# Optimization experiments

Hardware: AMD Instinct MI355X
Metric: run time of the kernel (lower is better)

Reference implementation:

```python
import jax, jax.numpy as jnp
import numpy as np

B, C, E, H = 4, 2048, 1024, 16
D = E // H
EPS = 1e-5

def _layernorm(x, g, b):
    mu = jnp.mean(x, axis=-1, keepdims=True)
    var = jnp.mean(jnp.square(x - mu), axis=-1, keepdims=True)
    return (x - mu) * jax.lax.rsqrt(var + EPS) * g + b

def setup_inputs() -> dict:
    key = jax.random.key(0)
    ks = jax.random.split(key, 12)
    s = 1.0 / np.sqrt(E)
    return {
        "inputs": jax.random.normal(ks[0], (B, C, E), dtype=jnp.float32),
        "Wq": jax.random.normal(ks[1], (E, E), dtype=jnp.float32) * s,
        "bq": jnp.zeros((E,), dtype=jnp.float32),
        "Wk": jax.random.normal(ks[2], (E, E), dtype=jnp.float32) * s,
        "bk": jnp.zeros((E,), dtype=jnp.float32),
        "Wv": jax.random.normal(ks[3], (E, E), dtype=jnp.float32) * s,
        "bv": jnp.zeros((E,), dtype=jnp.float32),
        "g1": jnp.ones((E,), dtype=jnp.float32),
        "beta1": jnp.zeros((E,), dtype=jnp.float32),
        "g2": jnp.ones((E,), dtype=jnp.float32),
        "beta2": jnp.zeros((E,), dtype=jnp.float32),
        "W1": jax.random.normal(ks[4], (E, 4 * E), dtype=jnp.float32) * s,
        "bm1": jnp.zeros((4 * E,), dtype=jnp.float32),
        "W2": jax.random.normal(ks[5], (4 * E, E), dtype=jnp.float32) * (1.0 / np.sqrt(4 * E)),
        "bm2": jnp.zeros((E,), dtype=jnp.float32),
    }

def reference(inputs, Wq, bq, Wk, bk, Wv, bv, g1, beta1, g2, beta2, W1, bm1, W2, bm2):
    b, c, e = inputs.shape
    normed = _layernorm(inputs, g1, beta1)
    q = (normed @ Wq + bq).reshape(b, c, H, D).transpose(0, 2, 1, 3)  # [B,H,C,D]
    k = (normed @ Wk + bk).reshape(b, c, H, D).transpose(0, 2, 1, 3)
    v = (normed @ Wv + bv).reshape(b, c, H, D).transpose(0, 2, 1, 3)
    scores = jnp.einsum('bhqd,bhkd->bhqk', q, k) / np.sqrt(D).astype(np.float32)
    causal = jnp.triu(jnp.ones((c, c), dtype=bool), k=1)  # True above diagonal
    scores = jnp.where(causal, -jnp.inf, scores)
    probs = jax.nn.softmax(scores, axis=-1)
    attn = jnp.einsum('bhqk,bhkd->bhqd', probs, v)
    attn = attn.transpose(0, 2, 1, 3).reshape(b, c, e)
    out = inputs + attn
    h = _layernorm(out, g2, beta2)
    mlp = jax.nn.relu(h @ W1 + bm1) @ W2 + bm2
    return out + mlp
```

## Files before the change

kernel.cpp:

```cpp
#include <hip/hip_runtime.h>
#include <math.h>

#define B_ 4
#define C_ 2048
#define E_ 1024
#define H_ 16
#define D_ 64
#define ROWS_ (B_*C_)

typedef __bf16 bf16x8 __attribute__((ext_vector_type(8)));
typedef float f32x4 __attribute__((ext_vector_type(4)));

__device__ __forceinline__ float b2f(unsigned short u) {
  unsigned int x = ((unsigned int)u) << 16;
  return __builtin_bit_cast(float, x);
}
__device__ __forceinline__ unsigned short f2b(float f) {
  unsigned int x = __builtin_bit_cast(unsigned int, f);
  unsigned int r = (x + 0x7FFFu + ((x >> 16) & 1u)) >> 16;
  return (unsigned short)r;
}
__device__ __forceinline__ unsigned short tob(float f) { return f2b(f); }
__device__ __forceinline__ unsigned short tob(unsigned short u) { return u; }
__device__ __forceinline__ void store_out(float* p, float v) { *p = v; }
__device__ __forceinline__ void store_out(unsigned short* p, float v) { *p = f2b(v); }

__device__ __forceinline__ void async16(const void* g, void* l) {
  __builtin_amdgcn_global_load_lds(
      (__attribute__((address_space(1))) unsigned int*)g,
      (__attribute__((address_space(3))) unsigned int*)l, 16, 0, 0);
}

template <typename InT>
__global__ __launch_bounds__(256) void transpose64(
    const InT* __restrict__ in, unsigned short* __restrict__ out,
    int s_in, int s_out, int Hz, long zs_b, long zs_h, long zs_out)
{
  __shared__ unsigned short t[64][65];
  int z = blockIdx.z;
  long ib = (long)(z / Hz) * zs_b + (long)(z % Hz) * zs_h;
  long ob = (long)z * zs_out;
  int r0 = blockIdx.y * 64, c0 = blockIdx.x * 64;
  int lane = threadIdx.x & 63, grp = threadIdx.x >> 6;
  for (int i = grp; i < 64; i += 4)
    t[i][lane] = tob(in[ib + (long)(r0 + i) * s_in + c0 + lane]);
  __syncthreads();
  for (int i = grp; i < 64; i += 4)
    out[ob + (long)(c0 + i) * s_out + r0 + lane] = t[lane][i];
}

__global__ void concat_bias(const float* __restrict__ q,
                            const float* __restrict__ k,
                            const float* __restrict__ v,
                            float* __restrict__ o)
{
  int i = blockIdx.x * 256 + threadIdx.x;
  o[i] = (i < 1024) ? q[i] : (i < 2048) ? k[i - 1024] : v[i - 2048];
}

__global__ __launch_bounds__(256) void ln_kernel(
    const float* __restrict__ xin, const unsigned short* __restrict__ addend,
    const float* __restrict__ g, const float* __restrict__ beta,
    unsigned short* __restrict__ yout, float* __restrict__ out1)
{
  int row = blockIdx.x, tid = threadIdx.x;
  size_t base = (size_t)row * E_ + tid * 4;
  float4 xa = *(const float4*)(xin + base);
  float v0 = xa.x, v1 = xa.y, v2 = xa.z, v3 = xa.w;
  if (addend) {
    ushort4 aa = *(const ushort4*)(addend + base);
    v0 += b2f(aa.x); v1 += b2f(aa.y); v2 += b2f(aa.z); v3 += b2f(aa.w);
  }
  if (out1) {
    *(float4*)(out1 + base) = make_float4(v0, v1, v2, v3);
  }
  float s = v0 + v1 + v2 + v3;
  float sq = v0*v0 + v1*v1 + v2*v2 + v3*v3;
  #pragma unroll
  for (int off = 32; off >= 1; off >>= 1) {
    s  += __shfl_xor(s, off);
    sq += __shfl_xor(sq, off);
  }
  __shared__ float red[8];
  int wid = tid >> 6;
  if ((tid & 63) == 0) { red[wid] = s; red[4 + wid] = sq; }
  __syncthreads();
  s  = red[0] + red[1] + red[2] + red[3];
  sq = red[4] + red[5] + red[6] + red[7];
  float mu = s * (1.0f / E_);
  float var = sq * (1.0f / E_) - mu * mu;
  float rs = rsqrtf(var + 1e-5f);
  float4 ga = *(const float4*)(g + tid * 4);
  float4 ba = *(const float4*)(beta + tid * 4);
  ushort4 o;
  o.x = f2b((v0 - mu) * rs * ga.x + ba.x);
  o.y = f2b((v1 - mu) * rs * ga.y + ba.y);
  o.z = f2b((v2 - mu) * rs * ga.z + ba.z);
  o.w = f2b((v3 - mu) * rs * ga.w + ba.w);
  *(ushort4*)(yout + base) = o;
}

#define BARC() { asm volatile("" ::: "memory"); __builtin_amdgcn_s_barrier(); asm volatile("" ::: "memory"); }
#define WAITL() { asm volatile("s_waitcnt lgkmcnt(0)" ::: "memory"); __builtin_amdgcn_sched_barrier(0); }

#define MFMA16(mh, BF) do {                                                 \
  __builtin_amdgcn_s_setprio(1);                                            \
  _Pragma("unroll")                                                         \
  for (int mt_ = 0; mt_ < 4; ++mt_)                                         \
    _Pragma("unroll")                                                       \
    for (int nt_ = 0; nt_ < 4; ++nt_)                                       \
      acc[(mh)*4+mt_][nt_] = __builtin_amdgcn_mfma_f32_16x16x32_bf16(       \
          af[mt_], BF[nt_], acc[(mh)*4+mt_][nt_], 0, 0, 0);                 \
  __builtin_amdgcn_s_setprio(0);                                            \
} while (0)

template <typename OutT>
__global__ __launch_bounds__(512, 2) void gemm256(
    const unsigned short* __restrict__ A, const unsigned short* __restrict__ Bt,
    const float* __restrict__ bias, const float* __restrict__ resid,
    OutT* __restrict__ Co, int M, int N, int K, int lda, int ldb,
    int relu, size_t zs)
{
  __shared__ __align__(16) unsigned short As[2][256 * 64];
  __shared__ __align__(16) unsigned short Bs[2][256 * 64];
  int tid = threadIdx.x, lane = tid & 63, wid = tid >> 6;
  int lane15 = lane & 15, quad = lane >> 4;
  int wm = wid >> 2, wn = wid & 3;

  int i = blockIdx.x;
  int xcd = i & 7, c = i >> 3;
  int bm = xcd * 4 + (c & 3);
  int bn = c >> 2;
  size_t koff = (size_t)blockIdx.z * K;
  int z0 = (blockIdx.z == 0);
  Co += (size_t)blockIdx.z * zs;

  int sr = tid >> 3, sc = tid & 7;
  int gcol = (sc ^ (sr & 7)) * 8;
  const unsigned short* Ag = A + koff + (size_t)(bm * 256 + sr) * lda + gcol;
  const unsigned short* Bg = Bt + koff + (size_t)(bn * 256 + sr) * ldb + gcol;
  int dst = tid * 8;

  int NT = K >> 6;

  f32x4 acc[8][4];
  #pragma unroll
  for (int m = 0; m < 8; ++m)
    #pragma unroll
    for (int n = 0; n < 4; ++n) acc[m][n] = 0.0f;

  auto stA = [&](int kt, int h) {
    const unsigned short* s = Ag + (size_t)(h * 128) * lda + kt * 64;
    unsigned short* d = &As[kt & 1][h * 8192] + dst;
    async16(s, d);
    async16(s + (size_t)64 * lda, d + 4096);
  };
  auto stB = [&](int kt, int h) {
    const unsigned short* s = Bg + (size_t)(h * 128) * ldb + kt * 64;
    unsigned short* d = &Bs[kt & 1][h * 8192] + dst;
    async16(s, d);
    async16(s + (size_t)64 * ldb, d + 4096);
  };
  int rsw = lane15 & 7;
  auto ldA = [&](int q, int mh, int m, int kk) {
    return *(const bf16x8*)&As[q][(wm * 128 + mh * 64 + m * 16 + lane15) * 64
                                  + (((kk * 4 + quad) ^ rsw) * 8)];
  };
  auto ldB = [&](int q, int n, int kk) {
    return *(const bf16x8*)&Bs[q][(wn * 64 + n * 16 + lane15) * 64
                                  + (((kk * 4 + quad) ^ rsw) * 8)];
  };

  stB(0, 0); stB(0, 1); stA(0, 0); stA(0, 1);
  stB(1, 0); stB(1, 1);
  asm volatile("s_waitcnt vmcnt(4)" ::: "memory");
  __builtin_amdgcn_s_barrier();

  #pragma unroll 1
  for (int it = 0; it < (NT >> 1); ++it) {
    int u = 2 * it;
    bool more = (u + 2 < NT);
    bf16x8 af[4], b0[4], b1[4];

    #pragma unroll
    for (int n = 0; n < 4; ++n) b0[n] = ldB(0, n, 0);
    #pragma unroll
    for (int n = 0; n < 4; ++n) b1[n] = ldB(0, n, 1);
    #pragma unroll
    for (int m = 0; m < 4; ++m) af[m] = ldA(0, 0, m, 0);
    stA(u + 1, 0);
    BARC(); WAITL();
    MFMA16(0, b0);
    BARC();
    #pragma unroll
    for (int m = 0; m < 4; ++m) af[m] = ldA(0, 1, m, 0);
    stA(u + 1, 1);
    BARC(); WAITL();
    MFMA16(1, b0);
    BARC();
    #pragma unroll
    for (int m = 0; m < 4; ++m) af[m] = ldA(0, 0, m, 1);
    if (more) stB(u + 2, 0);
    BARC(); WAITL();
    MFMA16(0, b1);
    BARC();
    #pragma unroll
    for (int m = 0; m < 4; ++m) af[m] = ldA(0, 1, m, 1);
    if (more) stB(u + 2, 1);
    BARC(); WAITL();
    MFMA16(1, b1);
    if (more) { asm volatile("s_waitcnt vmcnt(4)" ::: "memory"); }
    else      { asm volatile("s_waitcnt vmcnt(0)" ::: "memory"); }
    BARC();

    #pragma unroll
    for (int n = 0; n < 4; ++n) b0[n] = ldB(1, n, 0);
    #pragma unroll
    for (int n = 0; n < 4; ++n) b1[n] = ldB(1, n, 1);
    #pragma unroll
    for (int m = 0; m < 4; ++m) af[m] = ldA(1, 0, m, 0);
    if (more) stA(u + 2, 0);
    BARC(); WAITL();
    MFMA16(0, b0);
    BARC();
    #pragma unroll
    for (int m = 0; m < 4; ++m) af[m] = ldA(1, 1, m, 0);
    if (more) stA(u + 2, 1);
    BARC(); WAITL();
    MFMA16(1, b0);
    BARC();
    #pragma unroll
    for (int m = 0; m < 4; ++m) af[m] = ldA(1, 0, m, 1);
    if (more) stB(u + 3, 0);
    BARC(); WAITL();
    MFMA16(0, b1);
    BARC();
    #pragma unroll
    for (int m = 0; m < 4; ++m) af[m] = ldA(1, 1, m, 1);
    if (more) stB(u + 3, 1);
    BARC(); WAITL();
    MFMA16(1, b1);
    if (more) { asm volatile("s_waitcnt vmcnt(4)" ::: "memory"); }
    BARC();
  }

  #pragma unroll
  for (int nt = 0; nt < 4; ++nt) {
    int col = bn * 256 + wn * 64 + nt * 16 + lane15;
    float bv = (bias && z0) ? bias[col] : 0.0f;
    #pragma unroll
    for (int mt = 0; mt < 8; ++mt) {
      int row0 = bm * 256 + wm * 128 + mt * 16 + quad * 4;
      #pragma unroll
      for (int r = 0; r < 4; ++r) {
        float val = acc[mt][nt][r] + bv;
        if (relu) val = fmaxf(val, 0.0f);
        if (resid && z0) val += resid[(size_t)(row0 + r) * N + col];
        store_out(&Co[(size_t)(row0 + r) * N + col], val);
      }
    }
  }
}

__global__ __launch_bounds__(256) void add2(
    const float* __restrict__ p0, const float* __restrict__ p1,
    float* __restrict__ out)
{
  size_t i = ((size_t)blockIdx.x * 256 + threadIdx.x) * 4;
  float4 a = *(const float4*)(p0 + i);
  float4 b = *(const float4*)(p1 + i);
  *(float4*)(out + i) = make_float4(a.x + b.x, a.y + b.y, a.z + b.z, a.w + b.w);
}

__global__ __launch_bounds__(512) void attn_kernel(
    const unsigned short* __restrict__ qkv, const unsigned short* __restrict__ vt,
    unsigned short* __restrict__ attnb,
    float* __restrict__ opart0, float* __restrict__ opart1,
    float* __restrict__ lpart)
{
  __shared__ __align__(16) unsigned short Klds[64 * 64];
  __shared__ __align__(16) unsigned short Vlds[64 * 64];
  __shared__ __align__(16) unsigned short Plds[8][16 * 72];
  int tid = threadIdx.x, lane = tid & 63, widx = tid >> 6;
  int lane15 = lane & 15, quad = lane >> 4;

  int bx = blockIdx.x;
  int qblk, p, split;
  if (bx < 16) { qblk = 15 - (bx >> 1); p = bx & 1; split = 1; }
  else         { qblk = 23 - bx;        p = 0;      split = 0; }
  int ntiles = 2 * qblk + 2;
  int kt0 = (split && p) ? (qblk + 1) : 0;
  int kt1 = (split && !p) ? (qblk + 1) : ntiles;

  int bh = blockIdx.y;
  int b = bh >> 4, h = bh & 15;
  int q0w = qblk * 128 + widx * 16;

  const float QSCALE = 0.18033688011112042f;
  const unsigned short* qb = qkv + (size_t)(b * C_ + q0w + lane15) * 3072 + h * 64;
  bf16x8 qa0 = *(const bf16x8*)(qb + quad * 8);
  bf16x8 qa1 = *(const bf16x8*)(qb + 32 + quad * 8);
  #pragma unroll
  for (int j = 0; j < 8; ++j) {
    qa0[j] = (__bf16)((float)qa0[j] * QSCALE);
    qa1[j] = (__bf16)((float)qa1[j] * QSCALE);
  }

  float lsum[4];
  f32x4 o[4];
  #pragma unroll
  for (int r = 0; r < 4; ++r) lsum[r] = 0.0f;
  #pragma unroll
  for (int nt = 0; nt < 4; ++nt) o[nt] = 0.0f;

  int sr = tid >> 3, sc = tid & 7, sw = sr & 7;
  const unsigned short* kg = qkv + (size_t)(b * C_ + kt0 * 64 + sr) * 3072 + 1024 + h * 64 + (sc ^ sw) * 8;
  const unsigned short* vg = vt + (size_t)bh * 64 * 2048 + (size_t)sr * 2048 + (sc ^ sw) * 8 + kt0 * 64;
  unsigned short* kl = &Klds[sr * 64 + sc * 8];
  unsigned short* vl = &Vlds[sr * 64 + sc * 8];
  int swr = lane15 & 7;

  for (int kt = kt0; kt < kt1; ++kt) {
    int k0 = kt * 64;
    async16(kg, kl);
    async16(vg, vl);
    kg += (size_t)64 * 3072;
    vg += 64;
    __syncthreads();

    if (k0 <= q0w + 15) {
      f32x4 s[4];
      #pragma unroll
      for (int g = 0; g < 4; ++g) s[g] = 0.0f;
      #pragma unroll
      for (int g = 0; g < 4; ++g) {
        int row = g * 16 + lane15;
        bf16x8 kf0 = *(const bf16x8*)&Klds[row * 64 + ((quad ^ swr) * 8)];
        bf16x8 kf1 = *(const bf16x8*)&Klds[row * 64 + (((4 + quad) ^ swr) * 8)];
        s[g] = __builtin_amdgcn_mfma_f32_16x16x32_bf16(qa0, kf0, s[g], 0, 0, 0);
        s[g] = __builtin_amdgcn_mfma_f32_16x16x32_bf16(qa1, kf1, s[g], 0, 0, 0);
      }

      if (k0 + 63 > q0w) {
        #pragma unroll
        for (int g = 0; g < 4; ++g)
          #pragma unroll
          for (int r = 0; r < 4; ++r)
            if (k0 + g * 16 + lane15 > q0w + quad * 4 + r) s[g][r] = -3.0e38f;
      }

      float pv[4][4];
      #pragma unroll
      for (int g = 0; g < 4; ++g)
        #pragma unroll
        for (int r = 0; r < 4; ++r) pv[g][r] = exp2f(s[g][r]);
      #pragma unroll
      for (int r = 0; r < 4; ++r)
        lsum[r] += (pv[0][r] + pv[1][r]) + (pv[2][r] + pv[3][r]);

      __bf16* prow = (__bf16*)&Plds[widx][0];
      #pragma unroll
      for (int g = 0; g < 4; ++g)
        #pragma unroll
        for (int r = 0; r < 4; ++r)
          prow[(quad * 4 + r) * 72 + g * 16 + lane15] = (__bf16)pv[g][r];
      asm volatile("s_waitcnt lgkmcnt(0)" ::: "memory");
      bf16x8 pa0 = *(const bf16x8*)&Plds[widx][lane15 * 72 + quad * 8];
      bf16x8 pa1 = *(const bf16x8*)&Plds[widx][lane15 * 72 + 32 + quad * 8];

      #pragma unroll
      for (int nt = 0; nt < 4; ++nt) {
        int d = nt * 16 + lane15;
        bf16x8 vf0 = *(const bf16x8*)&Vlds[d * 64 + ((quad ^ swr) * 8)];
        bf16x8 vf1 = *(const bf16x8*)&Vlds[d * 64 + (((4 + quad) ^ swr) * 8)];
        o[nt] = __builtin_amdgcn_mfma_f32_16x16x32_bf16(pa0, vf0, o[nt], 0, 0, 0);
        o[nt] = __builtin_amdgcn_mfma_f32_16x16x32_bf16(pa1, vf1, o[nt], 0, 0, 0);
      }
    }
    __syncthreads();
  }

  #pragma unroll
  for (int off = 1; off <= 8; off <<= 1)
    #pragma unroll
    for (int r = 0; r < 4; ++r)
      lsum[r] += __shfl_xor(lsum[r], off);

  if (!split) {
    float rl[4];
    #pragma unroll
    for (int r = 0; r < 4; ++r) rl[r] = 1.0f / lsum[r];
    #pragma unroll
    for (int nt = 0; nt < 4; ++nt)
      #pragma unroll
      for (int r = 0; r < 4; ++r) {
        float val = o[nt][r] * rl[r];
        attnb[(size_t)(b * C_ + q0w + quad * 4 + r) * E_ + h * 64 + nt * 16 + lane15] = f2b(val);
      }
  } else {
    float* op = p ? opart1 : opart0;
    size_t rbase = (size_t)bh * 1024 + (q0w - 1024) + quad * 4;
    #pragma unroll
    for (int nt = 0; nt < 4; ++nt)
      #pragma unroll
      for (int r = 0; r < 4; ++r)
        op[(rbase + r) * 64 + nt * 16 + lane15] = o[nt][r];
    if (lane15 == 0) {
      float* lp = lpart + (size_t)p * 65536;
      #pragma unroll
      for (int r = 0; r < 4; ++r) lp[rbase + r] = lsum[r];
    }
  }
}

__global__ __launch_bounds__(256) void attn_combine(
    const float* __restrict__ opart0, const float* __restrict__ opart1,
    const float* __restrict__ lpart, unsigned short* __restrict__ attnb)
{
  size_t i = (size_t)blockIdx.x * 256 + threadIdx.x;
  int d = (int)(i & 63);
  size_t rowi = i >> 6;
  int bh = (int)(rowi >> 10), row = (int)(rowi & 1023);
  float ov = opart0[rowi * 64 + d] + opart1[rowi * 64 + d];
  float lv = lpart[rowi] + lpart[65536 + rowi];
  int b = bh >> 4, h = bh & 15;
  attnb[(size_t)(b * C_ + 1024 + row) * E_ + h * 64 + d] = f2b(ov / lv);
}

extern "C" void kernel_launch(void* const* d_in, const int* in_sizes, int n_in,
                              void* d_out, int out_size, void* d_ws, size_t ws_size,
                              hipStream_t stream)
{
  const float* x   = (const float*)d_in[0];
  const float* Wq  = (const float*)d_in[1];
  const float* bq  = (const float*)d_in[2];
  const float* Wk  = (const float*)d_in[3];
  const float* bk  = (const float*)d_in[4];
  const float* Wv  = (const float*)d_in[5];
  const float* bv  = (const float*)d_in[6];
  const float* g1  = (const float*)d_in[7];
  const float* be1 = (const float*)d_in[8];
  const float* g2  = (const float*)d_in[9];
  const float* be2 = (const float*)d_in[10];
  const float* W1  = (const float*)d_in[11];
  const float* bm1 = (const float*)d_in[12];
  const float* W2  = (const float*)d_in[13];
  const float* bm2 = (const float*)d_in[14];

  char* ws = (char*)d_ws;
  float*          part0 = (float*)(ws + 0);
  unsigned short* norm1 = (unsigned short*)(ws + 0);
  unsigned short* wT    = (unsigned short*)(ws + 16777216);
  unsigned short* w1T   = (unsigned short*)(ws + 23068672);
  float*          biasq = (float*)(ws + 39845888);
  unsigned short* qkv   = (unsigned short*)(ws + 39858176);
  unsigned short* vtb   = (unsigned short*)(ws + 90189824);
  unsigned short* mid   = (unsigned short*)(ws + 39858176);
  unsigned short* attnb = (unsigned short*)(ws + 106967040);
  float*          out1  = (float*)(ws + 123744256);
  unsigned short* w2T   = (unsigned short*)(ws + 157298688);
  float*          part1 = (float*)(ws + 165687296);
  float*          opart0 = (float*)(ws + 165687296);
  float*          opart1 = (float*)(ws + 123744256);
  float*          lpartb = (float*)(ws + 0);
  size_t part_zs = ((size_t)165687296) / 4;

  transpose64<float><<<dim3(16, 16, 1), 256, 0, stream>>>(Wq, wT,               1024, 1024, 1, 0, 0, 0);
  transpose64<float><<<dim3(16, 16, 1), 256, 0, stream>>>(Wk, wT + 1024 * 1024, 1024, 1024, 1, 0, 0, 0);
  transpose64<float><<<dim3(16, 16, 1), 256, 0, stream>>>(Wv, wT + 2048 * 1024, 1024, 1024, 1, 0, 0, 0);
  transpose64<float><<<dim3(64, 16, 1), 256, 0, stream>>>(W1, w1T, 4096, 1024, 1, 0, 0, 0);
  transpose64<float><<<dim3(16, 64, 1), 256, 0, stream>>>(W2, w2T, 1024, 4096, 1, 0, 0, 0);
  concat_bias<<<12, 256, 0, stream>>>(bq, bk, bv, biasq);

  ln_kernel<<<ROWS_, 256, 0, stream>>>(x, nullptr, g1, be1, norm1, nullptr);

  gemm256<unsigned short><<<dim3(384, 1, 1), 512, 0, stream>>>(
      norm1, wT, biasq, nullptr, qkv, 8192, 3072, 1024, 1024, 1024, 0, 0);

  transpose64<unsigned short><<<dim3(1, 32, 64), 256, 0, stream>>>(
      qkv + 2048, vtb, 3072, 2048, 16, (long)C_ * 3072, 64, (long)64 * 2048);

  attn_kernel<<<dim3(24, 64), 512, 0, stream>>>(qkv, vtb, attnb, opart0, opart1, lpartb);
  attn_combine<<<16384, 256, 0, stream>>>(opart0, opart1, lpartb, attnb);

  ln_kernel<<<ROWS_, 256, 0, stream>>>(x, attnb, g2, be2, norm1, out1);

  gemm256<unsigned short><<<dim3(512, 1, 1), 512, 0, stream>>>(
      norm1, w1T, bm1, nullptr, mid, 8192, 4096, 1024, 1024, 1024, 1, 0);

  gemm256<float><<<dim3(128, 1, 2), 512, 0, stream>>>(
      mid, w2T, bm2, out1, part0, 8192, 1024, 2048, 4096, 4096, 0, part_zs);
  add2<<<8192, 256, 0, stream>>>(part0, part1, (float*)d_out);
}
```

Baseline: 561.1 us.

## Double-buffer K/V tiles in attention kernel with async prefetch

Adds a second LDS buffer for the K and V tiles and issues the async global-to-LDS load for the next tile before computing on the current one. Partial vmcnt waits and raw s_barrier replace the full __syncthreads, so load latency can overlap with the MFMA and softmax work. This doubles K/V LDS use, which may lower occupancy, and it relies on the vmcnt accounting being correct.

```diff
diff --git a/kernel.cpp b/kernel.cpp
--- a/kernel.cpp
+++ b/kernel.cpp
@@ -278,8 +278,8 @@
     float* __restrict__ opart0, float* __restrict__ opart1,
     float* __restrict__ lpart)
 {
-  __shared__ __align__(16) unsigned short Klds[64 * 64];
-  __shared__ __align__(16) unsigned short Vlds[64 * 64];
+  __shared__ __align__(16) unsigned short Klds[2][64 * 64];
+  __shared__ __align__(16) unsigned short Vlds[2][64 * 64];
   __shared__ __align__(16) unsigned short Plds[8][16 * 72];
   int tid = threadIdx.x, lane = tid & 63, widx = tid >> 6;
   int lane15 = lane & 15, quad = lane >> 4;
@@ -316,17 +316,30 @@
   int sr = tid >> 3, sc = tid & 7, sw = sr & 7;
   const unsigned short* kg = qkv + (size_t)(b * C_ + kt0 * 64 + sr) * 3072 + 1024 + h * 64 + (sc ^ sw) * 8;
   const unsigned short* vg = vt + (size_t)bh * 64 * 2048 + (size_t)sr * 2048 + (sc ^ sw) * 8 + kt0 * 64;
-  unsigned short* kl = &Klds[sr * 64 + sc * 8];
-  unsigned short* vl = &Vlds[sr * 64 + sc * 8];
+  unsigned short* kl = &Klds[0][sr * 64 + sc * 8];
+  unsigned short* vl = &Vlds[0][sr * 64 + sc * 8];
   int swr = lane15 & 7;
 
+  async16(kg, kl);
+  async16(vg, vl);
+  kg += (size_t)64 * 3072;
+  vg += 64;
+
   for (int kt = kt0; kt < kt1; ++kt) {
+    int cur = (kt - kt0) & 1;
     int k0 = kt * 64;
-    async16(kg, kl);
-    async16(vg, vl);
-    kg += (size_t)64 * 3072;
-    vg += 64;
-    __syncthreads();
+    bool morek = (kt + 1 < kt1);
+    if (morek) {
+      async16(kg, kl + (cur ^ 1) * 4096);
+      async16(vg, vl + (cur ^ 1) * 4096);
+      kg += (size_t)64 * 3072;
+      vg += 64;
+      asm volatile("s_waitcnt vmcnt(2)" ::: "memory");
+    } else {
+      asm volatile("s_waitcnt vmcnt(0)" ::: "memory");
+    }
+    __builtin_amdgcn_s_barrier();
+    asm volatile("" ::: "memory");
 
     if (k0 <= q0w + 15) {
       f32x4 s[4];
@@ -335,8 +348,8 @@
       #pragma unroll
       for (int g = 0; g < 4; ++g) {
         int row = g * 16 + lane15;
-        bf16x8 kf0 = *(const bf16x8*)&Klds[row * 64 + ((quad ^ swr) * 8)];
-        bf16x8 kf1 = *(const bf16x8*)&Klds[row * 64 + (((4 + quad) ^ swr) * 8)];
+        bf16x8 kf0 = *(const bf16x8*)&Klds[cur][row * 64 + ((quad ^ swr) * 8)];
+        bf16x8 kf1 = *(const bf16x8*)&Klds[cur][row * 64 + (((4 + quad) ^ swr) * 8)];
         s[g] = __builtin_amdgcn_mfma_f32_16x16x32_bf16(qa0, kf0, s[g], 0, 0, 0);
         s[g] = __builtin_amdgcn_mfma_f32_16x16x32_bf16(qa1, kf1, s[g], 0, 0, 0);
       }
@@ -371,13 +384,15 @@
       #pragma unroll
       for (int nt = 0; nt < 4; ++nt) {
         int d = nt * 16 + lane15;
-        bf16x8 vf0 = *(const bf16x8*)&Vlds[d * 64 + ((quad ^ swr) * 8)];
-        bf16x8 vf1 = *(const bf16x8*)&Vlds[d * 64 + (((4 + quad) ^ swr) * 8)];
+        bf16x8 vf0 = *(const bf16x8*)&Vlds[cur][d * 64 + ((quad ^ swr) * 8)];
+        bf16x8 vf1 = *(const bf16x8*)&Vlds[cur][d * 64 + (((4 + quad) ^ swr) * 8)];
         o[nt] = __builtin_amdgcn_mfma_f32_16x16x32_bf16(pa0, vf0, o[nt], 0, 0, 0);
         o[nt] = __builtin_amdgcn_mfma_f32_16x16x32_bf16(pa1, vf1, o[nt], 0, 0, 0);
       }
     }
-    __syncthreads();
+    asm volatile("" ::: "memory");
+    __builtin_amdgcn_s_barrier();
+    asm volatile("" ::: "memory");
   }
 
   #pragma unroll
```

After: 564.4 us. Within noise of the previous version (+0.6%).
